# Optimization experiments

Hardware: AMD Instinct MI355X
Metric: run time of the kernel (lower is better)

The kernel has to match this reference:

```python
import jax, jax.numpy as jnp
import numpy as np

N_NODES = 100000
N_EDGES = 600000
D = 128


def setup_inputs() -> dict:
    key = jax.random.key(0)
    k_h, k_ei, k_ea, k_wm, k_bm, k_wu, k_bu = jax.random.split(key, 7)
    h = jax.random.normal(k_h, (N_NODES, D), dtype=jnp.float32)
    edge_index = jax.random.randint(k_ei, (2, N_EDGES), 0, N_NODES, dtype=jnp.int64)
    edge_attr = jax.random.normal(k_ea, (N_EDGES, D), dtype=jnp.float32)
    # nn.Linear params (W stored as [out, in] in torch; keep [in, out] here)
    s_m = 1.0 / np.sqrt(3 * D)
    s_u = 1.0 / np.sqrt(2 * D)
    W_msg = jax.random.uniform(k_wm, (3 * D, D), jnp.float32, -s_m, s_m)
    b_msg = jax.random.uniform(k_bm, (D,), jnp.float32, -s_m, s_m)
    W_upd = jax.random.uniform(k_wu, (2 * D, D), jnp.float32, -s_u, s_u)
    b_upd = jax.random.uniform(k_bu, (D,), jnp.float32, -s_u, s_u)
    return {"h": h, "edge_index": edge_index, "edge_attr": edge_attr,
            "W_msg": W_msg, "b_msg": b_msg, "W_upd": W_upd, "b_upd": b_upd}


def reference(h, edge_index, edge_attr, W_msg, b_msg, W_upd, b_upd):
    send, rec = edge_index[0], edge_index[1]
    h_send = h[send]                      # [E, D] gather
    h_rec = h[rec]                        # [E, D] gather
    msg_in = jnp.concatenate((h_send, h_rec, edge_attr), axis=1)  # [E, 3D]
    messages = msg_in @ W_msg + b_msg     # [E, D]
    messages_agg = jax.ops.segment_sum(messages, rec, num_segments=h.shape[0])  # [N, D]
    upd_in = jnp.concatenate((h, messages_agg), axis=1)           # [N, 2D]
    out = upd_in @ W_upd + b_upd          # [N, D]
    return out
```

## Files before the change

### kernel.cpp

```cpp
#include <hip/hip_runtime.h>

#define N_NODES 100000
#define N_EDGES 600000
#define D 128
#define MAXDEG 64
#define OVF_CAP 4096
#define BM 16

typedef __attribute__((ext_vector_type(8))) short bf16x8;
typedef __attribute__((ext_vector_type(4))) float f32x4;

static __device__ inline ushort f2bf(float f) {
    unsigned x = __float_as_uint(f);
    unsigned r = (x + 0x7fffu + ((x >> 16) & 1u)) >> 16;
    return (ushort)r;
}
static __device__ inline f32x4 nt_load4(const float* p) {
    return __builtin_nontemporal_load((const f32x4*)p);
}
static __device__ inline ushort4 pack4(f32x4 v) {
    ushort4 u;
    u.x = f2bf(v[0]); u.y = f2bf(v[1]); u.z = f2bf(v[2]); u.w = f2bf(v[3]);
    return u;
}


__global__ void k_zero(int* __restrict__ cnt) {
    int i = blockIdx.x * 256 + threadIdx.x;
    if (i < N_NODES + 1) cnt[i] = 0;
}

__global__ void k_build_w(const float* __restrict__ W_msg,
                          const float* __restrict__ b_msg,
                          const float* __restrict__ W_upd,
                          ushort* __restrict__ Wfrag,
                          float* __restrict__ Wcat32,
                          float* __restrict__ bv)
{
    int gid = blockIdx.x * 256 + threadIdx.x;
    if (gid < 512 * 128) {
        int i = gid & 7;
        int l = (gid >> 3) & 63;
        int fb = gid >> 9;
        int kb = fb >> 3, cb = fb & 7;
        int k = kb * 32 + ((l >> 4) * 8) + i;
        int j = cb * 16 + (l & 15);
        float acc;
        if (k < 128) {
            acc = W_upd[k * 128 + j];
        } else {
            int r = k - 128;
            acc = 0.f;
            #pragma unroll 4
            for (int dd = 0; dd < 128; ++dd)
                acc += W_msg[r * 128 + dd] * W_upd[(128 + dd) * 128 + j];
        }
        Wfrag[gid] = f2bf(acc);
        Wcat32[k * 128 + j] = acc;
    } else if (gid < 512 * 128 + 128) {
        int j = gid - 512 * 128;
        float acc = 0.f;
        for (int dd = 0; dd < 128; ++dd)
            acc += b_msg[dd] * W_upd[(128 + dd) * 128 + j];
        bv[j] = acc;
    }
}

__global__ void k_bucket(const int* __restrict__ eidx,
                         int* __restrict__ cnt,
                         int* __restrict__ ovf,
                         int2* __restrict__ elist2)
{
    int e = blockIdx.x * 256 + threadIdx.x;
    if (e >= N_EDGES) return;
    int s = eidx[e];
    int r = eidx[N_EDGES + e];
    int slot = atomicAdd(cnt + r, 1);
    if (slot < MAXDEG) {
        elist2[(size_t)r * MAXDEG + slot] = make_int2(e, s);
    } else {
        int p = atomicAdd(cnt + N_NODES, 1);
        if (p < OVF_CAP) ovf[p] = e;
    }
}

__global__ __launch_bounds__(256, 8) void k_fused(
    const float* __restrict__ h,
    const float* __restrict__ ea,
    const int* __restrict__ cnt,
    const int2* __restrict__ elist2,
    const ushort* __restrict__ Wfrag,
    const float* __restrict__ bv,
    const float* __restrict__ b_upd,
    float* __restrict__ out)
{
    __shared__ ushort Xs[BM][520];
    __shared__ float degL[BM];
    const int tid = threadIdx.x;
    const int lane = tid & 63;
    const int half = lane >> 5;
    const int hl = lane & 31;
    const int wv = tid >> 6;
    const int n0 = blockIdx.x * BM;
    const int nb = n0 + wv * 4;

    int2 es = elist2[(size_t)nb * MAXDEG + lane];
    int   c = cnt[nb];

    for (int u = 0; u < 4; ++u) {
        const int i = wv * 4 + u;
        const int n = nb + u;
        int2 es_n; int c_n;
        if (u < 3) {
            es_n = elist2[(size_t)(n + 1) * MAXDEG + lane];
            c_n  = cnt[n + 1];
        }
        const int m = c < MAXDEG ? c : MAXDEG;

        f32x4 aS = {0.f, 0.f, 0.f, 0.f};
        f32x4 aE = {0.f, 0.f, 0.f, 0.f};
        int t = 0;
        for (; t + 4 <= m; t += 4) {
            int iA = t + half, iB = t + 2 + half;
            int eA = __shfl(es.x, iA), sA = __shfl(es.y, iA);
            int eB = __shfl(es.x, iB), sB = __shfl(es.y, iB);
            f32x4 a0 = *(const f32x4*)(h + (size_t)sA * D + hl * 4);
            f32x4 b0 = nt_load4(ea + (size_t)eA * D + hl * 4);
            f32x4 a1 = *(const f32x4*)(h + (size_t)sB * D + hl * 4);
            f32x4 b1 = nt_load4(ea + (size_t)eB * D + hl * 4);
            aS += a0 + a1;
            aE += b0 + b1;
        }
        for (; t < m; t += 2) {
            int idx = t + half;
            if (idx < m) {
                int eA = __shfl(es.x, idx), sA = __shfl(es.y, idx);
                f32x4 a0 = *(const f32x4*)(h + (size_t)sA * D + hl * 4);
                f32x4 b0 = nt_load4(ea + (size_t)eA * D + hl * 4);
                aS += a0;
                aE += b0;
            }
        }
        aS[0] += __shfl_xor(aS[0], 32); aS[1] += __shfl_xor(aS[1], 32);
        aS[2] += __shfl_xor(aS[2], 32); aS[3] += __shfl_xor(aS[3], 32);
        aE[0] += __shfl_xor(aE[0], 32); aE[1] += __shfl_xor(aE[1], 32);
        aE[2] += __shfl_xor(aE[2], 32); aE[3] += __shfl_xor(aE[3], 32);

        const float dv = (float)c;
        f32x4 hn = *(const f32x4*)(h + (size_t)n * D + hl * 4);
        if (half == 0) {
            *(ushort4*)&Xs[i][      hl * 4] = pack4(hn);
            *(ushort4*)&Xs[i][128 + hl * 4] = pack4(aS);
        } else {
            f32x4 dh = {dv * hn[0], dv * hn[1], dv * hn[2], dv * hn[3]};
            *(ushort4*)&Xs[i][256 + hl * 4] = pack4(dh);
            *(ushort4*)&Xs[i][384 + hl * 4] = pack4(aE);
        }
        if (lane == 0) degL[i] = dv;
        es = es_n; c = c_n;
    }
    __syncthreads();

    const int arow = lane & 15;
    const int koff = (lane >> 4) * 8;

    f32x4 acc[2] = {};
    for (int kb = 0; kb < 16; ++kb) {
        bf16x8 a = *(const bf16x8*)&Xs[arow][kb * 32 + koff];
        #pragma unroll
        for (int cc = 0; cc < 2; ++cc) {
            int fb = kb * 8 + wv * 2 + cc;
            bf16x8 b = *(const bf16x8*)(Wfrag + ((size_t)fb * 64 + lane) * 8);
            acc[cc] = __builtin_amdgcn_mfma_f32_16x16x32_bf16(a, b, acc[cc], 0, 0, 0);
        }
    }

    const int r0 = (lane >> 4) * 4;
    #pragma unroll
    for (int cc = 0; cc < 2; ++cc) {
        int col = wv * 32 + cc * 16 + (lane & 15);
        float bvv = bv[col];
        float buv = b_upd[col];
        #pragma unroll
        for (int r = 0; r < 4; ++r) {
            int rl = r0 + r;
            out[(size_t)(n0 + rl) * D + col] = acc[cc][r] + degL[rl] * bvv + buv;
        }
    }
}

__global__ void k_ovf(const float* __restrict__ h,
                      const int* __restrict__ eidx,
                      const float* __restrict__ ea,
                      const int* __restrict__ cnt,
                      const int* __restrict__ ovf,
                      const float* __restrict__ Wcat32,
                      float* __restrict__ out)
{
    int ncnt = cnt[N_NODES];
    if (ncnt > OVF_CAP) ncnt = OVF_CAP;
    if (ncnt <= 0) return;
    int lane = threadIdx.x & 63;
    int w = threadIdx.x >> 6;
    for (int i = w; i < ncnt; i += 4) {
        int e = ovf[i];
        int s = eidx[e];
        int r = eidx[N_EDGES + e];
        float acc0 = 0.f, acc1 = 0.f;
        for (int dd = 0; dd < 128; ++dd) {
            float hs = h[(size_t)s * D + dd];
            float ev = ea[(size_t)e * D + dd];
            acc0 += hs * Wcat32[(128 + dd) * 128 + lane * 2]     + ev * Wcat32[(384 + dd) * 128 + lane * 2];
            acc1 += hs * Wcat32[(128 + dd) * 128 + lane * 2 + 1] + ev * Wcat32[(384 + dd) * 128 + lane * 2 + 1];
        }
        atomicAdd(out + (size_t)r * D + lane * 2 + 0, acc0);
        atomicAdd(out + (size_t)r * D + lane * 2 + 1, acc1);
    }
}

extern "C" void kernel_launch(void* const* d_in, const int* in_sizes, int n_in,
                              void* d_out, int out_size, void* d_ws, size_t ws_size,
                              hipStream_t stream)
{
    const float* h     = (const float*)d_in[0];
    const int*   eidx  = (const int*)d_in[1];
    const float* eattr = (const float*)d_in[2];
    const float* W_msg = (const float*)d_in[3];
    const float* b_msg = (const float*)d_in[4];
    const float* W_upd = (const float*)d_in[5];
    const float* b_upd = (const float*)d_in[6];
    float* out = (float*)d_out;

    char* base = (char*)d_ws;
    ushort* Wfrag  = (ushort*)(base);
    float*  Wcat32 = (float*)(base + 131072);
    float*  bv     = (float*)(base + 393216);
    int*    cnt    = (int*)(base + 393728);
    int*    ovf    = (int*)(base + 794736);
    int2*   elist2 = (int2*)(base + 811120);

    k_zero<<<(N_NODES + 1 + 255) / 256, 256, 0, stream>>>(cnt);
    k_build_w<<<(512 * 128 + 128 + 255) / 256, 256, 0, stream>>>(W_msg, b_msg, W_upd, Wfrag, Wcat32, bv);
    k_bucket<<<(N_EDGES + 255) / 256, 256, 0, stream>>>(eidx, cnt, ovf, elist2);
    k_fused<<<N_NODES / BM, 256, 0, stream>>>(h, eattr, cnt, elist2, Wfrag, bv, b_upd, out);
    k_ovf<<<1, 256, 0, stream>>>(h, eidx, eattr, cnt, ovf, Wcat32, out);
}
```

Before: 172.1 us.

## Split fused gather+GEMM into separate gather and GEMM kernels

The fused kernel is split into two. k_gather3 assigns one half-wave per node, sums the gathered sender features and edge attributes, and writes them as bf16 into a workspace buffer together with the degree. k_gemm then loads h and those sums into shared memory and runs the MFMA GEMM. The aim is to decouple the latency-bound gather from the GEMM so each kernel gets its own occupancy and parallelism, at the cost of an extra global round trip (about 51 MB) and one more kernel launch.

```diff
diff --git a/kernel.cpp b/kernel.cpp
--- a/kernel.cpp
+++ b/kernel.cpp
@@ -84,11 +84,67 @@
     }
 }
 
-__global__ __launch_bounds__(256, 8) void k_fused(
+__global__ __launch_bounds__(256, 8) void k_gather3(
     const float* __restrict__ h,
     const float* __restrict__ ea,
     const int* __restrict__ cnt,
     const int2* __restrict__ elist2,
+    ushort* __restrict__ Sea16,
+    float* __restrict__ deg)
+{
+    int gid = blockIdx.x * 256 + threadIdx.x;
+    int w = gid >> 6;
+    if (w >= N_NODES / 2) return;
+    const int lane = gid & 63;
+    const int half = lane >> 5;
+    const int hl = lane & 31;
+    const int n = 2 * w + half;
+
+    const int c = cnt[n];
+    const int m = c < MAXDEG ? c : MAXDEG;
+    int2 es = elist2[(size_t)n * MAXDEG + hl];
+
+    f32x4 aS = {0.f, 0.f, 0.f, 0.f};
+    f32x4 aE = {0.f, 0.f, 0.f, 0.f};
+    int t = 0;
+    for (; t + 2 <= m; t += 2) {
+        int e0, s0, e1, s1;
+        if (t + 1 < 32) {
+            e0 = __shfl(es.x, half * 32 + t);     s0 = __shfl(es.y, half * 32 + t);
+            e1 = __shfl(es.x, half * 32 + t + 1); s1 = __shfl(es.y, half * 32 + t + 1);
+        } else {
+            int2 p0 = elist2[(size_t)n * MAXDEG + t];
+            int2 p1 = elist2[(size_t)n * MAXDEG + t + 1];
+            e0 = p0.x; s0 = p0.y; e1 = p1.x; s1 = p1.y;
+        }
+        f32x4 a0 = *(const f32x4*)(h + (size_t)s0 * D + hl * 4);
+        f32x4 b0 = nt_load4(ea + (size_t)e0 * D + hl * 4);
+        f32x4 a1 = *(const f32x4*)(h + (size_t)s1 * D + hl * 4);
+        f32x4 b1 = nt_load4(ea + (size_t)e1 * D + hl * 4);
+        aS += a0 + a1;
+        aE += b0 + b1;
+    }
+    if (t < m) {
+        int e0, s0;
+        if (t < 32) {
+            e0 = __shfl(es.x, half * 32 + t); s0 = __shfl(es.y, half * 32 + t);
+        } else {
+            int2 p0 = elist2[(size_t)n * MAXDEG + t];
+            e0 = p0.x; s0 = p0.y;
+        }
+        aS += *(const f32x4*)(h + (size_t)s0 * D + hl * 4);
+        aE += nt_load4(ea + (size_t)e0 * D + hl * 4);
+    }
+
+    *(ushort4*)(Sea16 + (size_t)n * 256 +       hl * 4) = pack4(aS);
+    *(ushort4*)(Sea16 + (size_t)n * 256 + 128 + hl * 4) = pack4(aE);
+    if (hl == 0) deg[n] = (float)c;
+}
+
+__global__ __launch_bounds__(256, 8) void k_gemm(
+    const float* __restrict__ h,
+    const ushort* __restrict__ Sea16,
+    const float* __restrict__ deg,
     const ushort* __restrict__ Wfrag,
     const float* __restrict__ bv,
     const float* __restrict__ b_upd,
@@ -97,70 +153,36 @@
     __shared__ ushort Xs[BM][520];
     __shared__ float degL[BM];
     const int tid = threadIdx.x;
+    const int n0 = blockIdx.x * BM;
+    if (tid < BM) degL[tid] = deg[n0 + tid];
+
+    for (int q = tid; q < BM * 64; q += 256) {
+        int i = q >> 6, j = q & 63;
+        int n = n0 + i;
+        if (j < 16) {
+            f32x4 v0 = *(const f32x4*)(h + (size_t)n * D + j * 8);
+            f32x4 v1 = *(const f32x4*)(h + (size_t)n * D + j * 8 + 4);
+            *(ushort4*)&Xs[i][j * 8]     = pack4(v0);
+            *(ushort4*)&Xs[i][j * 8 + 4] = pack4(v1);
+        } else if (j < 32) {
+            uint4 v = *(const uint4*)(Sea16 + (size_t)n * 256 + (j - 16) * 8);
+            *(uint4*)&Xs[i][j * 8] = v;
+        } else if (j < 48) {
+            float dv = deg[n];
+            f32x4 v0 = *(const f32x4*)(h + (size_t)n * D + (j - 32) * 8);
+            f32x4 v1 = *(const f32x4*)(h + (size_t)n * D + (j - 32) * 8 + 4);
+            v0 *= dv; v1 *= dv;
+            *(ushort4*)&Xs[i][j * 8]     = pack4(v0);
+            *(ushort4*)&Xs[i][j * 8 + 4] = pack4(v1);
+        } else {
+            uint4 v = *(const uint4*)(Sea16 + (size_t)n * 256 + 128 + (j - 48) * 8);
+            *(uint4*)&Xs[i][j * 8] = v;
+        }
+    }
+    __syncthreads();
+
     const int lane = tid & 63;
-    const int half = lane >> 5;
-    const int hl = lane & 31;
     const int wv = tid >> 6;
-    const int n0 = blockIdx.x * BM;
-    const int nb = n0 + wv * 4;
-
-    int2 es = elist2[(size_t)nb * MAXDEG + lane];
-    int   c = cnt[nb];
-
-    for (int u = 0; u < 4; ++u) {
-        const int i = wv * 4 + u;
-        const int n = nb + u;
-        int2 es_n; int c_n;
-        if (u < 3) {
-            es_n = elist2[(size_t)(n + 1) * MAXDEG + lane];
-            c_n  = cnt[n + 1];
-        }
-        const int m = c < MAXDEG ? c : MAXDEG;
-
-        f32x4 aS = {0.f, 0.f, 0.f, 0.f};
-        f32x4 aE = {0.f, 0.f, 0.f, 0.f};
-        int t = 0;
-        for (; t + 4 <= m; t += 4) {
-            int iA = t + half, iB = t + 2 + half;
-            int eA = __shfl(es.x, iA), sA = __shfl(es.y, iA);
-            int eB = __shfl(es.x, iB), sB = __shfl(es.y, iB);
-            f32x4 a0 = *(const f32x4*)(h + (size_t)sA * D + hl * 4);
-            f32x4 b0 = nt_load4(ea + (size_t)eA * D + hl * 4);
-            f32x4 a1 = *(const f32x4*)(h + (size_t)sB * D + hl * 4);
-            f32x4 b1 = nt_load4(ea + (size_t)eB * D + hl * 4);
-            aS += a0 + a1;
-            aE += b0 + b1;
-        }
-        for (; t < m; t += 2) {
-            int idx = t + half;
-            if (idx < m) {
-                int eA = __shfl(es.x, idx), sA = __shfl(es.y, idx);
-                f32x4 a0 = *(const f32x4*)(h + (size_t)sA * D + hl * 4);
-                f32x4 b0 = nt_load4(ea + (size_t)eA * D + hl * 4);
-                aS += a0;
-                aE += b0;
-            }
-        }
-        aS[0] += __shfl_xor(aS[0], 32); aS[1] += __shfl_xor(aS[1], 32);
-        aS[2] += __shfl_xor(aS[2], 32); aS[3] += __shfl_xor(aS[3], 32);
-        aE[0] += __shfl_xor(aE[0], 32); aE[1] += __shfl_xor(aE[1], 32);
-        aE[2] += __shfl_xor(aE[2], 32); aE[3] += __shfl_xor(aE[3], 32);
-
-        const float dv = (float)c;
-        f32x4 hn = *(const f32x4*)(h + (size_t)n * D + hl * 4);
-        if (half == 0) {
-            *(ushort4*)&Xs[i][      hl * 4] = pack4(hn);
-            *(ushort4*)&Xs[i][128 + hl * 4] = pack4(aS);
-        } else {
-            f32x4 dh = {dv * hn[0], dv * hn[1], dv * hn[2], dv * hn[3]};
-            *(ushort4*)&Xs[i][256 + hl * 4] = pack4(dh);
-            *(ushort4*)&Xs[i][384 + hl * 4] = pack4(aE);
-        }
-        if (lane == 0) degL[i] = dv;
-        es = es_n; c = c_n;
-    }
-    __syncthreads();
-
     const int arow = lane & 15;
     const int koff = (lane >> 4) * 8;
 
@@ -235,13 +257,16 @@
     ushort* Wfrag  = (ushort*)(base);
     float*  Wcat32 = (float*)(base + 131072);
     float*  bv     = (float*)(base + 393216);
-    int*    cnt    = (int*)(base + 393728);
-    int*    ovf    = (int*)(base + 794736);
-    int2*   elist2 = (int2*)(base + 811120);
+    float*  deg    = (float*)(base + 393728);
+    int*    cnt    = (int*)(base + 793728);
+    int*    ovf    = (int*)(base + 1193744);
+    int2*   elist2 = (int2*)(base + 1210128);
+    ushort* Sea16  = (ushort*)(base + 52410128);
 
     k_zero<<<(N_NODES + 1 + 255) / 256, 256, 0, stream>>>(cnt);
     k_build_w<<<(512 * 128 + 128 + 255) / 256, 256, 0, stream>>>(W_msg, b_msg, W_upd, Wfrag, Wcat32, bv);
     k_bucket<<<(N_EDGES + 255) / 256, 256, 0, stream>>>(eidx, cnt, ovf, elist2);
-    k_fused<<<N_NODES / BM, 256, 0, stream>>>(h, eattr, cnt, elist2, Wfrag, bv, b_upd, out);
+    k_gather3<<<(N_NODES / 2 * 64) / 256, 256, 0, stream>>>(h, eattr, cnt, elist2, Sea16, deg);
+    k_gemm<<<N_NODES / BM, 256, 0, stream>>>(h, Sea16, deg, Wfrag, bv, b_upd, out);
     k_ovf<<<1, 256, 0, stream>>>(h, eidx, eattr, cnt, ovf, Wcat32, out);
 }
```

Measured after the change: 204.6 us. +18.9%, slower.

## Pre-sort edge attributes into per-receiver bf16 slots and gather bf16 node features

Applied to the files above, without the earlier changes.

The bucketing kernel now also converts each edge's attribute row to bf16 and writes it into a contiguous per-receiver slot array. A new kernel converts h to bf16, so the fused kernel gathers half-width rows and streams edge attributes contiguously instead of gathering them per edge id. MAXDEG drops from 64 to 32 to shrink the padded slot arrays. The cost is an extra full read of edge_attr plus a bf16 write and re-read, an extra pass over h, and earlier bf16 rounding of the inputs to the aggregation sums.

```diff
diff --git a/kernel.cpp b/kernel.cpp
--- a/kernel.cpp
+++ b/kernel.cpp
@@ -3,20 +3,21 @@
 #define N_NODES 100000
 #define N_EDGES 600000
 #define D 128
-#define MAXDEG 64
+#define MAXDEG 32
 #define OVF_CAP 4096
 #define BM 16
 
 typedef __attribute__((ext_vector_type(8))) short bf16x8;
 typedef __attribute__((ext_vector_type(4))) float f32x4;
+typedef __attribute__((ext_vector_type(2))) float f32x2;
 
 static __device__ inline ushort f2bf(float f) {
     unsigned x = __float_as_uint(f);
     unsigned r = (x + 0x7fffu + ((x >> 16) & 1u)) >> 16;
     return (ushort)r;
 }
-static __device__ inline f32x4 nt_load4(const float* p) {
-    return __builtin_nontemporal_load((const f32x4*)p);
+static __device__ inline float bf2f(ushort u) {
+    return __uint_as_float((unsigned)u << 16);
 }
 static __device__ inline ushort4 pack4(f32x4 v) {
     ushort4 u;
@@ -66,29 +67,59 @@
     }
 }
 
-__global__ void k_bucket(const int* __restrict__ eidx,
-                         int* __restrict__ cnt,
-                         int* __restrict__ ovf,
-                         int2* __restrict__ elist2)
-{
-    int e = blockIdx.x * 256 + threadIdx.x;
-    if (e >= N_EDGES) return;
-    int s = eidx[e];
-    int r = eidx[N_EDGES + e];
-    int slot = atomicAdd(cnt + r, 1);
-    if (slot < MAXDEG) {
-        elist2[(size_t)r * MAXDEG + slot] = make_int2(e, s);
-    } else {
-        int p = atomicAdd(cnt + N_NODES, 1);
-        if (p < OVF_CAP) ovf[p] = e;
+__global__ void k_hcvt(const float* __restrict__ h, ushort* __restrict__ h16) {
+    int gid = blockIdx.x * 256 + threadIdx.x;
+    if (gid >= N_NODES * D / 4) return;
+    f32x4 v = *(const f32x4*)(h + (size_t)gid * 4);
+    *(ushort4*)(h16 + (size_t)gid * 4) = pack4(v);
+}
+
+__global__ __launch_bounds__(256, 8) void k_bucketcvt(
+    const int* __restrict__ eidx,
+    const float* __restrict__ ea,
+    int* __restrict__ cnt,
+    int* __restrict__ ovf,
+    int* __restrict__ sendid,
+    ushort* __restrict__ easrt16)
+{
+    __shared__ int sLDS[256];
+    const int tid = threadIdx.x;
+    const int e0 = blockIdx.x * 256;
+    const int e = e0 + tid;
+
+    int dst = -1;
+    if (e < N_EDGES) {
+        int s = eidx[e];
+        int r = eidx[N_EDGES + e];
+        int slot = atomicAdd(cnt + r, 1);
+        if (slot < MAXDEG) {
+            dst = r * MAXDEG + slot;
+            sendid[dst] = s;
+        } else {
+            int p = atomicAdd(cnt + N_NODES, 1);
+            if (p < OVF_CAP) ovf[p] = e;
+        }
+    }
+    sLDS[tid] = dst;
+    __syncthreads();
+
+    const int lane = tid & 63;
+    const int w = tid >> 6;
+    for (int i = 0; i < 64; ++i) {
+        int d = sLDS[w * 64 + i];
+        if (d < 0) continue;
+        int ee = e0 + w * 64 + i;
+        f32x2 v = __builtin_nontemporal_load((const f32x2*)(ea + (size_t)ee * D + lane * 2));
+        ushort2 u; u.x = f2bf(v[0]); u.y = f2bf(v[1]);
+        *(ushort2*)(easrt16 + (size_t)d * D + lane * 2) = u;
     }
 }
 
 __global__ __launch_bounds__(256, 8) void k_fused(
-    const float* __restrict__ h,
-    const float* __restrict__ ea,
+    const ushort* __restrict__ h16,
     const int* __restrict__ cnt,
-    const int2* __restrict__ elist2,
+    const int* __restrict__ sendid,
+    const ushort* __restrict__ easrt16,
     const ushort* __restrict__ Wfrag,
     const float* __restrict__ bv,
     const float* __restrict__ b_upd,
@@ -104,41 +135,54 @@
     const int n0 = blockIdx.x * BM;
     const int nb = n0 + wv * 4;
 
-    int2 es = elist2[(size_t)nb * MAXDEG + lane];
-    int   c = cnt[nb];
+    int sid = sendid[(size_t)nb * MAXDEG + (lane & 31)];
+    int c = cnt[nb];
 
     for (int u = 0; u < 4; ++u) {
         const int i = wv * 4 + u;
         const int n = nb + u;
-        int2 es_n; int c_n;
+        int sid_n; int c_n;
         if (u < 3) {
-            es_n = elist2[(size_t)(n + 1) * MAXDEG + lane];
+            sid_n = sendid[(size_t)(n + 1) * MAXDEG + (lane & 31)];
             c_n  = cnt[n + 1];
         }
         const int m = c < MAXDEG ? c : MAXDEG;
+        const ushort* erow = easrt16 + (size_t)n * MAXDEG * D;
 
         f32x4 aS = {0.f, 0.f, 0.f, 0.f};
         f32x4 aE = {0.f, 0.f, 0.f, 0.f};
         int t = 0;
         for (; t + 4 <= m; t += 4) {
             int iA = t + half, iB = t + 2 + half;
-            int eA = __shfl(es.x, iA), sA = __shfl(es.y, iA);
-            int eB = __shfl(es.x, iB), sB = __shfl(es.y, iB);
-            f32x4 a0 = *(const f32x4*)(h + (size_t)sA * D + hl * 4);
-            f32x4 b0 = nt_load4(ea + (size_t)eA * D + hl * 4);
-            f32x4 a1 = *(const f32x4*)(h + (size_t)sB * D + hl * 4);
-            f32x4 b1 = nt_load4(ea + (size_t)eB * D + hl * 4);
-            aS += a0 + a1;
-            aE += b0 + b1;
+            int sA = __shfl(sid, iA);
+            int sB = __shfl(sid, iB);
+            uint2 a0 = *(const uint2*)(h16 + (size_t)sA * D + hl * 4);
+            uint2 b0 = *(const uint2*)(erow + (size_t)iA * D + hl * 4);
+            uint2 a1 = *(const uint2*)(h16 + (size_t)sB * D + hl * 4);
+            uint2 b1 = *(const uint2*)(erow + (size_t)iB * D + hl * 4);
+            aS[0] += bf2f((ushort)a0.x) + bf2f((ushort)a1.x);
+            aS[1] += bf2f((ushort)(a0.x >> 16)) + bf2f((ushort)(a1.x >> 16));
+            aS[2] += bf2f((ushort)a0.y) + bf2f((ushort)a1.y);
+            aS[3] += bf2f((ushort)(a0.y >> 16)) + bf2f((ushort)(a1.y >> 16));
+            aE[0] += bf2f((ushort)b0.x) + bf2f((ushort)b1.x);
+            aE[1] += bf2f((ushort)(b0.x >> 16)) + bf2f((ushort)(b1.x >> 16));
+            aE[2] += bf2f((ushort)b0.y) + bf2f((ushort)b1.y);
+            aE[3] += bf2f((ushort)(b0.y >> 16)) + bf2f((ushort)(b1.y >> 16));
         }
         for (; t < m; t += 2) {
             int idx = t + half;
             if (idx < m) {
-                int eA = __shfl(es.x, idx), sA = __shfl(es.y, idx);
-                f32x4 a0 = *(const f32x4*)(h + (size_t)sA * D + hl * 4);
-                f32x4 b0 = nt_load4(ea + (size_t)eA * D + hl * 4);
-                aS += a0;
-                aE += b0;
+                int sA = __shfl(sid, idx);
+                uint2 a0 = *(const uint2*)(h16 + (size_t)sA * D + hl * 4);
+                uint2 b0 = *(const uint2*)(erow + (size_t)idx * D + hl * 4);
+                aS[0] += bf2f((ushort)a0.x);
+                aS[1] += bf2f((ushort)(a0.x >> 16));
+                aS[2] += bf2f((ushort)a0.y);
+                aS[3] += bf2f((ushort)(a0.y >> 16));
+                aE[0] += bf2f((ushort)b0.x);
+                aE[1] += bf2f((ushort)(b0.x >> 16));
+                aE[2] += bf2f((ushort)b0.y);
+                aE[3] += bf2f((ushort)(b0.y >> 16));
             }
         }
         aS[0] += __shfl_xor(aS[0], 32); aS[1] += __shfl_xor(aS[1], 32);
@@ -147,17 +191,21 @@
         aE[2] += __shfl_xor(aE[2], 32); aE[3] += __shfl_xor(aE[3], 32);
 
         const float dv = (float)c;
-        f32x4 hn = *(const f32x4*)(h + (size_t)n * D + hl * 4);
+        uint2 hn2 = *(const uint2*)(h16 + (size_t)n * D + hl * 4);
         if (half == 0) {
-            *(ushort4*)&Xs[i][      hl * 4] = pack4(hn);
+            *(uint2*)&Xs[i][      hl * 4] = hn2;
             *(ushort4*)&Xs[i][128 + hl * 4] = pack4(aS);
         } else {
-            f32x4 dh = {dv * hn[0], dv * hn[1], dv * hn[2], dv * hn[3]};
+            f32x4 dh;
+            dh[0] = dv * bf2f((ushort)hn2.x);
+            dh[1] = dv * bf2f((ushort)(hn2.x >> 16));
+            dh[2] = dv * bf2f((ushort)hn2.y);
+            dh[3] = dv * bf2f((ushort)(hn2.y >> 16));
             *(ushort4*)&Xs[i][256 + hl * 4] = pack4(dh);
             *(ushort4*)&Xs[i][384 + hl * 4] = pack4(aE);
         }
         if (lane == 0) degL[i] = dv;
-        es = es_n; c = c_n;
+        sid = sid_n; c = c_n;
     }
     __syncthreads();
 
@@ -232,16 +280,19 @@
     float* out = (float*)d_out;
 
     char* base = (char*)d_ws;
-    ushort* Wfrag  = (ushort*)(base);
-    float*  Wcat32 = (float*)(base + 131072);
-    float*  bv     = (float*)(base + 393216);
-    int*    cnt    = (int*)(base + 393728);
-    int*    ovf    = (int*)(base + 794736);
-    int2*   elist2 = (int2*)(base + 811120);
+    ushort* Wfrag   = (ushort*)(base);
+    float*  Wcat32  = (float*)(base + 131072);
+    float*  bv      = (float*)(base + 393216);
+    int*    cnt     = (int*)(base + 393728);
+    int*    ovf     = (int*)(base + 793856);
+    int*    sendid  = (int*)(base + 810240);
+    ushort* easrt16 = (ushort*)(base + 13610240);
+    ushort* h16     = (ushort*)(base + 13610240 + (size_t)N_NODES * MAXDEG * D * 2);
 
     k_zero<<<(N_NODES + 1 + 255) / 256, 256, 0, stream>>>(cnt);
     k_build_w<<<(512 * 128 + 128 + 255) / 256, 256, 0, stream>>>(W_msg, b_msg, W_upd, Wfrag, Wcat32, bv);
-    k_bucket<<<(N_EDGES + 255) / 256, 256, 0, stream>>>(eidx, cnt, ovf, elist2);
-    k_fused<<<N_NODES / BM, 256, 0, stream>>>(h, eattr, cnt, elist2, Wfrag, bv, b_upd, out);
+    k_hcvt<<<(N_NODES * D / 4 + 255) / 256, 256, 0, stream>>>(h, h16);
+    k_bucketcvt<<<(N_EDGES + 255) / 256, 256, 0, stream>>>(eidx, eattr, cnt, ovf, sendid, easrt16);
+    k_fused<<<N_NODES / BM, 256, 0, stream>>>(h16, cnt, sendid, easrt16, Wfrag, bv, b_upd, out);
     k_ovf<<<1, 256, 0, stream>>>(h, eidx, eattr, cnt, ovf, Wcat32, out);
 }
```

After: 250.8 us. +45.7%, slower.
